# Kernel optimization log

Measured on AMD Instinct MI355X. Metric: run time of the kernel, lower is better.

The kernel has to match this reference:

```python
import jax, jax.numpy as jnp
import numpy as np

EMB_DIM = 768
NUM_HEADS = 12
OUT_DIM = 768


def setup_inputs() -> dict:
    key = jax.random.key(0)
    k_x, k_q, k_k, k_v, k_o = jax.random.split(key, 5)
    B, N, D = 8, 1024, EMB_DIM
    s = 1.0 / np.sqrt(D)
    return {
        "x": jax.random.normal(k_x, (B, N, D), dtype=jnp.float32),
        # torch nn.Linear weights are stored [out_features, in_features]
        "Wq": jax.random.normal(k_q, (D, D), dtype=jnp.float32) * s,
        "Wk": jax.random.normal(k_k, (D, D), dtype=jnp.float32) * s,
        "Wv": jax.random.normal(k_v, (D, D), dtype=jnp.float32) * s,
        "Wo": jax.random.normal(k_o, (OUT_DIM, D), dtype=jnp.float32) * s,
    }


def _split_heads(t, H):
    # [B, N, D] -> [B*H, N, D//H]  (heads folded into batch, per einsum 'b i d')
    B, N, D = t.shape
    return t.reshape(B, N, H, D // H).transpose(0, 2, 1, 3).reshape(B * H, N, D // H)


def _merge_heads(t, B, H):
    BH, N, dh = t.shape
    return t.reshape(B, H, N, dh).transpose(0, 2, 1, 3).reshape(B, N, H * dh)


def reference(x, Wq, Wk, Wv, Wo):
    B, N, D = x.shape
    H = NUM_HEADS
    dh = D // H
    # q/k/v projections (torch Linear: y = x @ W.T, no bias)
    q = _split_heads(x @ Wq.T, H)
    k = _split_heads(x @ Wk.T, H)
    v = _split_heads(x @ Wv.T, H)
    scale = dh ** (-0.5)
    # dots: 'b i d , b j d -> b i j' -> full [B*H, N, N] score matrix
    dots = jnp.einsum('bid,bjd->bij', q, k) * scale
    attn = jax.nn.softmax(dots, axis=-1)
    # dropout p=0.0 -> identity
    # vect: 'b i d , b d j -> b i j' == attn @ v
    vect = jnp.einsum('bij,bjd->bid', attn, v)
    out = _merge_heads(vect, B, H) @ Wo.T
    return out
```

## Files before the change

### kernel.cpp

```cpp
#include <hip/hip_runtime.h>
#include <hip/hip_bf16.h>
#include <stdint.h>


typedef __bf16 bf16x8 __attribute__((ext_vector_type(8)));
typedef float f32x4 __attribute__((ext_vector_type(4)));

#define GAS __attribute__((address_space(1)))
#define LAS __attribute__((address_space(3)))

__device__ __forceinline__ void glds16(const short* gp, short* lp) {
  __builtin_amdgcn_global_load_lds((const GAS void*)gp, (LAS void*)lp, 16, 0, 0);
}

__device__ __forceinline__ short f2bf_bits(float f) {
  union { float f; unsigned u; } cv; cv.f = f;
  unsigned u = cv.u;
  unsigned r = (u + 0x7fffu + ((u >> 16) & 1u)) >> 16;
  return (short)(unsigned short)r;
}

__device__ __forceinline__ void stage8_f32(const float* __restrict__ src, short* dst) {
  float4 f0 = ((const float4*)src)[0];
  float4 f1 = ((const float4*)src)[1];
  short t[8];
  t[0] = f2bf_bits(f0.x); t[1] = f2bf_bits(f0.y);
  t[2] = f2bf_bits(f0.z); t[3] = f2bf_bits(f0.w);
  t[4] = f2bf_bits(f1.x); t[5] = f2bf_bits(f1.y);
  t[6] = f2bf_bits(f1.z); t[7] = f2bf_bits(f1.w);
  *(uint4*)dst = *(const uint4*)t;
}

__global__ __launch_bounds__(256) void convert_kernel(
    const float* __restrict__ x, const float* __restrict__ Wq,
    const float* __restrict__ Wk, const float* __restrict__ Wv,
    short* __restrict__ xb, short* __restrict__ wqkv) {
  int seg = blockIdx.y;
  const float* src; short* dst; int n8;
  if (seg == 0) { src = x; dst = xb; n8 = 786432; }
  else {
    src = (seg == 1) ? Wq : (seg == 2) ? Wk : Wv;
    dst = wqkv + (size_t)(seg - 1) * 589824;
    n8 = 73728;
  }
  int idx = blockIdx.x * 256 + threadIdx.x;
  if (idx >= n8) return;
  stage8_f32(src + (size_t)idx * 8, dst + (size_t)idx * 8);
}

__global__ __launch_bounds__(256) void gemm_qkv(
    const short* __restrict__ xb, const short* __restrict__ wqkv,
    short* __restrict__ q, short* __restrict__ k, short* __restrict__ vt) {
  const int m0 = blockIdx.x * 128;
  const int by = blockIdx.y;
  const int n0g = by * 128;
  const int tid = threadIdx.x;
  const int w = tid >> 6, lane = tid & 63, l16 = lane & 15, quad = lane >> 4;
  const int wr = w >> 1, wc = w & 1;

  __shared__ short sA[128 * 64];
  __shared__ short sB[128 * 64];

  f32x4 acc[4][4];
#pragma unroll
  for (int i = 0; i < 4; ++i)
#pragma unroll
    for (int j = 0; j < 4; ++j) acc[i][j] = (f32x4){0.f, 0.f, 0.f, 0.f};

  for (int k0 = 0; k0 < 768; k0 += 64) {
    __syncthreads();
    const short* Ab = xb + (size_t)m0 * 768 + k0;
    const short* Bb = wqkv + (size_t)n0g * 768 + k0;
#pragma unroll
    for (int p = 0; p < 4; ++p) {
      int lin = (w * 4 + p) * 64 + lane;
      int row = lin >> 3;
      int cs = ((lin & 7) ^ (row & 7)) * 8;
      glds16(Ab + (size_t)row * 768 + cs, &sA[lin * 8]);
      glds16(Bb + (size_t)row * 768 + cs, &sB[lin * 8]);
    }
    __syncthreads();
#pragma unroll
    for (int kk2 = 0; kk2 < 2; ++kk2) {
      bf16x8 af[4], bfg[4];
#pragma unroll
      for (int t = 0; t < 4; ++t) {
        int ra = wr * 64 + t * 16 + l16;
        af[t] = *(const bf16x8*)&sA[ra * 64 + (((kk2 * 4 + quad) ^ (ra & 7)) << 3)];
        int rb = wc * 64 + t * 16 + l16;
        bfg[t] = *(const bf16x8*)&sB[rb * 64 + (((kk2 * 4 + quad) ^ (rb & 7)) << 3)];
      }
#pragma unroll
      for (int ti = 0; ti < 4; ++ti)
#pragma unroll
        for (int tj = 0; tj < 4; ++tj)
          acc[ti][tj] = __builtin_amdgcn_mfma_f32_16x16x32_bf16(af[ti], bfg[tj], acc[ti][tj], 0, 0, 0);
    }
  }

  const int wsel = by / 6;
  const int nl0 = (by % 6) * 128 + wc * 64;
  if (wsel == 2) {
#pragma unroll
    for (int ti = 0; ti < 4; ++ti)
#pragma unroll
      for (int tj = 0; tj < 4; ++tj) {
        int token = m0 + wr * 64 + ti * 16 + quad * 4;
        int nl = nl0 + tj * 16 + l16;
        int bh = (token >> 10) * 12 + (nl >> 6);
        short tmp[4];
#pragma unroll
        for (int r = 0; r < 4; ++r) tmp[r] = f2bf_bits(acc[ti][tj][r]);
        *(uint2*)(vt + (size_t)bh * 65536 + (size_t)(nl & 63) * 1024 + (token & 1023)) =
            *(const uint2*)tmp;
      }
  } else {
    short* C = wsel ? k : q;
#pragma unroll
    for (int ti = 0; ti < 4; ++ti)
#pragma unroll
      for (int tj = 0; tj < 4; ++tj)
#pragma unroll
        for (int r = 0; r < 4; ++r) {
          int row = m0 + wr * 64 + ti * 16 + quad * 4 + r;
          int nl = nl0 + tj * 16 + l16;
          C[(size_t)row * 768 + nl] = f2bf_bits(acc[ti][tj][r]);
        }
  }
}

__global__ __launch_bounds__(256) void attn_kernel(
    const short* __restrict__ q, const short* __restrict__ k,
    const short* __restrict__ vt, short* __restrict__ vect) {
  const int bh = blockIdx.y;
  const int b = bh / 12, h = bh % 12;
  const int m0 = blockIdx.x * 128;
  const int tid = threadIdx.x;
  const int w = tid >> 6, lane = tid & 63, l16 = lane & 15, quad = lane >> 4;

  __shared__ short sQ[128 * 64];
  __shared__ short sK[64 * 64];
  __shared__ short sVt[64 * 64];

  const size_t base = (size_t)b * 786432 + (size_t)h * 64;
  const size_t vbase = (size_t)bh * 65536;

#pragma unroll
  for (int p = 0; p < 4; ++p) {
    int lin = (w * 4 + p) * 64 + lane;
    int row = lin >> 3;
    int cs = ((lin & 7) ^ (row & 7)) * 8;
    glds16(q + base + (size_t)(m0 + row) * 768 + cs, &sQ[lin * 8]);
  }
  __syncthreads();
  bf16x8 bq[2][2];
#pragma unroll
  for (int g = 0; g < 2; ++g)
#pragma unroll
    for (int kk = 0; kk < 2; ++kk) {
      int row = w * 32 + g * 16 + l16;
      bq[g][kk] = *(const bf16x8*)&sQ[row * 64 + (((kk * 4 + quad) ^ (row & 7)) << 3)];
    }

  float l_acc[2] = {0.f, 0.f};
  f32x4 oacc[2][4];
#pragma unroll
  for (int g = 0; g < 2; ++g)
#pragma unroll
    for (int td = 0; td < 4; ++td) oacc[g][td] = (f32x4){0.f, 0.f, 0.f, 0.f};

  for (int j0 = 0; j0 < 1024; j0 += 64) {
    __syncthreads();
#pragma unroll
    for (int p = 0; p < 2; ++p) {
      int lin = (w * 2 + p) * 64 + lane;
      int row = lin >> 3;
      int cs = ((lin & 7) ^ (row & 7)) * 8;
      glds16(k + base + (size_t)(j0 + row) * 768 + cs, &sK[lin * 8]);
      glds16(vt + vbase + (size_t)row * 1024 + j0 + cs, &sVt[lin * 8]);
    }
    __syncthreads();

    f32x4 s[2][4];
#pragma unroll
    for (int g = 0; g < 2; ++g)
#pragma unroll
      for (int ti = 0; ti < 4; ++ti) s[g][ti] = (f32x4){0.f, 0.f, 0.f, 0.f};
#pragma unroll
    for (int kk = 0; kk < 2; ++kk)
#pragma unroll
      for (int ti = 0; ti < 4; ++ti) {
        int row = ti * 16 + l16;
        bf16x8 a = *(const bf16x8*)&sK[row * 64 + (((kk * 4 + quad) ^ (row & 7)) << 3)];
        s[0][ti] = __builtin_amdgcn_mfma_f32_16x16x32_bf16(a, bq[0][kk], s[0][ti], 0, 0, 0);
        s[1][ti] = __builtin_amdgcn_mfma_f32_16x16x32_bf16(a, bq[1][kk], s[1][ti], 0, 0, 0);
      }

    short ps[2][4][4];
#pragma unroll
    for (int g = 0; g < 2; ++g)
#pragma unroll
      for (int ti = 0; ti < 4; ++ti) {
        float p0 = __expf(s[g][ti][0] * 0.125f);
        float p1 = __expf(s[g][ti][1] * 0.125f);
        float p2 = __expf(s[g][ti][2] * 0.125f);
        float p3 = __expf(s[g][ti][3] * 0.125f);
        l_acc[g] += (p0 + p1) + (p2 + p3);
        ps[g][ti][0] = f2bf_bits(p0); ps[g][ti][1] = f2bf_bits(p1);
        ps[g][ti][2] = f2bf_bits(p2); ps[g][ti][3] = f2bf_bits(p3);
      }

#pragma unroll
    for (int t2 = 0; t2 < 2; ++t2) {
      bf16x8 av[4];
#pragma unroll
      for (int td = 0; td < 4; ++td) {
        int row = td * 16 + l16;
        int o1 = t2 * 32 + quad * 4;
        int c1 = o1 >> 3, w1 = o1 & 7;
        int c2 = c1 + 2;
        union { uint2 u[2]; bf16x8 v; } tmp;
        tmp.u[0] = *(const uint2*)&sVt[row * 64 + ((c1 ^ (row & 7)) << 3) + w1];
        tmp.u[1] = *(const uint2*)&sVt[row * 64 + ((c2 ^ (row & 7)) << 3) + w1];
        av[td] = tmp.v;
      }
#pragma unroll
      for (int g = 0; g < 2; ++g) {
        union { short sh[8]; bf16x8 v; } bp;
#pragma unroll
        for (int jj = 0; jj < 4; ++jj) {
          bp.sh[jj] = ps[g][2 * t2][jj];
          bp.sh[4 + jj] = ps[g][2 * t2 + 1][jj];
        }
#pragma unroll
        for (int td = 0; td < 4; ++td)
          oacc[g][td] = __builtin_amdgcn_mfma_f32_16x16x32_bf16(av[td], bp.v, oacc[g][td], 0, 0, 0);
      }
    }
  }

#pragma unroll
  for (int g = 0; g < 2; ++g) {
    float l = l_acc[g];
    l += __shfl_xor(l, 16);
    l += __shfl_xor(l, 32);
    float inv = 1.0f / l;
    int i_tok = m0 + w * 32 + g * 16 + l16;
#pragma unroll
    for (int td = 0; td < 4; ++td) {
      short tmp[4];
#pragma unroll
      for (int r = 0; r < 4; ++r) tmp[r] = f2bf_bits(oacc[g][td][r] * inv);
      *(uint2*)(vect + base + (size_t)i_tok * 768 + td * 16 + quad * 4) = *(const uint2*)tmp;
    }
  }
}

__global__ __launch_bounds__(256) void gemm_out(
    const short* __restrict__ vect, const float* __restrict__ Wo,
    float* __restrict__ out) {
  const int m0 = blockIdx.x * 128;
  const int n0 = blockIdx.y * 128;
  const int tid = threadIdx.x;
  const int w = tid >> 6, lane = tid & 63, l16 = lane & 15, quad = lane >> 4;
  const int wr = w >> 1, wc = w & 1;

  __shared__ short sA[128 * 64];
  __shared__ short sB[128 * 64];

  f32x4 acc[4][4];
#pragma unroll
  for (int i = 0; i < 4; ++i)
#pragma unroll
    for (int j = 0; j < 4; ++j) acc[i][j] = (f32x4){0.f, 0.f, 0.f, 0.f};

  for (int k0 = 0; k0 < 768; k0 += 64) {
    __syncthreads();
    const short* Ab = vect + (size_t)m0 * 768 + k0;
#pragma unroll
    for (int p = 0; p < 4; ++p) {
      int lin = (w * 4 + p) * 64 + lane;
      int row = lin >> 3;
      int cs = ((lin & 7) ^ (row & 7)) * 8;
      glds16(Ab + (size_t)row * 768 + cs, &sA[lin * 8]);
      stage8_f32(Wo + (size_t)(n0 + row) * 768 + k0 + cs, &sB[lin * 8]);
    }
    __syncthreads();
#pragma unroll
    for (int kk2 = 0; kk2 < 2; ++kk2) {
      bf16x8 af[4], bfg[4];
#pragma unroll
      for (int t = 0; t < 4; ++t) {
        int ra = wr * 64 + t * 16 + l16;
        af[t] = *(const bf16x8*)&sA[ra * 64 + (((kk2 * 4 + quad) ^ (ra & 7)) << 3)];
        int rb = wc * 64 + t * 16 + l16;
        bfg[t] = *(const bf16x8*)&sB[rb * 64 + (((kk2 * 4 + quad) ^ (rb & 7)) << 3)];
      }
#pragma unroll
      for (int ti = 0; ti < 4; ++ti)
#pragma unroll
        for (int tj = 0; tj < 4; ++tj)
          acc[ti][tj] = __builtin_amdgcn_mfma_f32_16x16x32_bf16(af[ti], bfg[tj], acc[ti][tj], 0, 0, 0);
    }
  }
#pragma unroll
  for (int ti = 0; ti < 4; ++ti)
#pragma unroll
    for (int tj = 0; tj < 4; ++tj)
#pragma unroll
      for (int r = 0; r < 4; ++r) {
        int row = m0 + wr * 64 + ti * 16 + quad * 4 + r;
        int col = n0 + wc * 64 + tj * 16 + l16;
        out[(size_t)row * 768 + col] = acc[ti][tj][r];
      }
}

extern "C" void kernel_launch(void* const* d_in, const int* in_sizes, int n_in,
                              void* d_out, int out_size, void* d_ws, size_t ws_size,
                              hipStream_t stream) {
  const float* x  = (const float*)d_in[0];
  const float* Wq = (const float*)d_in[1];
  const float* Wk = (const float*)d_in[2];
  const float* Wv = (const float*)d_in[3];
  const float* Wo = (const float*)d_in[4];
  float* out = (float*)d_out;

  const size_t MN = (size_t)8192 * 768;
  short* q    = (short*)d_ws;
  short* k    = q + MN;
  short* vt   = k + MN;
  short* vect = vt + MN;

  short* xb   = (short*)d_out;
  short* wqkv = xb + MN;

  convert_kernel<<<dim3(3072, 4), 256, 0, stream>>>(x, Wq, Wk, Wv, xb, wqkv);
  gemm_qkv<<<dim3(64, 18), 256, 0, stream>>>(xb, wqkv, q, k, vt);
  attn_kernel<<<dim3(8, 96), 256, 0, stream>>>(q, k, vt, vect);
  gemm_out<<<dim3(64, 6), 256, 0, stream>>>(vect, Wo, out);
}
```

Measured before the change: 208.9 us.

## Fold softmax scale into Q, use exp2, native bf16 converts, remap attention grid

Folds the softmax scale and log2(e) into the Q projection epilogue so the attention inner loop can call a raw exp2 builtin instead of a scaled __expf. It replaces the manual round-to-nearest bf16 bit trick with native __bf16 conversions, which may lower to hardware convert instructions. It also keeps the row-sum as a vector accumulator and makes the attention grid 1D with the head index varying fastest, which changes block scheduling and cache locality. Q is now stored pre-scaled in bf16, which slightly changes rounding. There is still no max subtraction, so the kernel relies on the scores being small.

```diff
diff --git a/kernel.cpp b/kernel.cpp
--- a/kernel.cpp
+++ b/kernel.cpp
@@ -4,6 +4,7 @@
 
 
 typedef __bf16 bf16x8 __attribute__((ext_vector_type(8)));
+typedef __bf16 bf16x4 __attribute__((ext_vector_type(4)));
 typedef float f32x4 __attribute__((ext_vector_type(4)));
 
 #define GAS __attribute__((address_space(1)))
@@ -13,22 +14,27 @@
   __builtin_amdgcn_global_load_lds((const GAS void*)gp, (LAS void*)lp, 16, 0, 0);
 }
 
-__device__ __forceinline__ short f2bf_bits(float f) {
-  union { float f; unsigned u; } cv; cv.f = f;
-  unsigned u = cv.u;
-  unsigned r = (u + 0x7fffu + ((u >> 16) & 1u)) >> 16;
-  return (short)(unsigned short)r;
+__device__ __forceinline__ float fast_exp2(float x) {
+#if __has_builtin(__builtin_amdgcn_exp2f)
+  return __builtin_amdgcn_exp2f(x);
+#else
+  return __expf(x * 0.6931471805599453f);
+#endif
+}
+
+__device__ __forceinline__ short bfbits(float f) {
+  __bf16 b = (__bf16)f;
+  union { __bf16 b; short s; } cv; cv.b = b;
+  return cv.s;
 }
 
 __device__ __forceinline__ void stage8_f32(const float* __restrict__ src, short* dst) {
   float4 f0 = ((const float4*)src)[0];
   float4 f1 = ((const float4*)src)[1];
-  short t[8];
-  t[0] = f2bf_bits(f0.x); t[1] = f2bf_bits(f0.y);
-  t[2] = f2bf_bits(f0.z); t[3] = f2bf_bits(f0.w);
-  t[4] = f2bf_bits(f1.x); t[5] = f2bf_bits(f1.y);
-  t[6] = f2bf_bits(f1.z); t[7] = f2bf_bits(f1.w);
-  *(uint4*)dst = *(const uint4*)t;
+  bf16x8 t;
+  t[0] = (__bf16)f0.x; t[1] = (__bf16)f0.y; t[2] = (__bf16)f0.z; t[3] = (__bf16)f0.w;
+  t[4] = (__bf16)f1.x; t[5] = (__bf16)f1.y; t[6] = (__bf16)f1.z; t[7] = (__bf16)f1.w;
+  *(bf16x8*)dst = t;
 }
 
 __global__ __launch_bounds__(256) void convert_kernel(
@@ -110,12 +116,13 @@
         int bh = (token >> 10) * 12 + (nl >> 6);
         short tmp[4];
 #pragma unroll
-        for (int r = 0; r < 4; ++r) tmp[r] = f2bf_bits(acc[ti][tj][r]);
+        for (int r = 0; r < 4; ++r) tmp[r] = bfbits(acc[ti][tj][r]);
         *(uint2*)(vt + (size_t)bh * 65536 + (size_t)(nl & 63) * 1024 + (token & 1023)) =
             *(const uint2*)tmp;
       }
   } else {
     short* C = wsel ? k : q;
+    const float sc = wsel ? 1.0f : 0.1803368801111244f;
 #pragma unroll
     for (int ti = 0; ti < 4; ++ti)
 #pragma unroll
@@ -124,7 +131,7 @@
         for (int r = 0; r < 4; ++r) {
           int row = m0 + wr * 64 + ti * 16 + quad * 4 + r;
           int nl = nl0 + tj * 16 + l16;
-          C[(size_t)row * 768 + nl] = f2bf_bits(acc[ti][tj][r]);
+          C[(size_t)row * 768 + nl] = bfbits(acc[ti][tj][r] * sc);
         }
   }
 }
@@ -132,9 +139,10 @@
 __global__ __launch_bounds__(256) void attn_kernel(
     const short* __restrict__ q, const short* __restrict__ k,
     const short* __restrict__ vt, short* __restrict__ vect) {
-  const int bh = blockIdx.y;
+  const int bh = blockIdx.x % 96;
+  const int qt = blockIdx.x / 96;
   const int b = bh / 12, h = bh % 12;
-  const int m0 = blockIdx.x * 128;
+  const int m0 = qt * 128;
   const int tid = threadIdx.x;
   const int w = tid >> 6, lane = tid & 63, l16 = lane & 15, quad = lane >> 4;
 
@@ -162,12 +170,14 @@
       bq[g][kk] = *(const bf16x8*)&sQ[row * 64 + (((kk * 4 + quad) ^ (row & 7)) << 3)];
     }
 
-  float l_acc[2] = {0.f, 0.f};
+  f32x4 l4[2];
   f32x4 oacc[2][4];
 #pragma unroll
-  for (int g = 0; g < 2; ++g)
+  for (int g = 0; g < 2; ++g) {
+    l4[g] = (f32x4){0.f, 0.f, 0.f, 0.f};
 #pragma unroll
     for (int td = 0; td < 4; ++td) oacc[g][td] = (f32x4){0.f, 0.f, 0.f, 0.f};
+  }
 
   for (int j0 = 0; j0 < 1024; j0 += 64) {
     __syncthreads();
@@ -196,18 +206,21 @@
         s[1][ti] = __builtin_amdgcn_mfma_f32_16x16x32_bf16(a, bq[1][kk], s[1][ti], 0, 0, 0);
       }
 
-    short ps[2][4][4];
+    bf16x4 pb[2][4];
 #pragma unroll
     for (int g = 0; g < 2; ++g)
 #pragma unroll
       for (int ti = 0; ti < 4; ++ti) {
-        float p0 = __expf(s[g][ti][0] * 0.125f);
-        float p1 = __expf(s[g][ti][1] * 0.125f);
-        float p2 = __expf(s[g][ti][2] * 0.125f);
-        float p3 = __expf(s[g][ti][3] * 0.125f);
-        l_acc[g] += (p0 + p1) + (p2 + p3);
-        ps[g][ti][0] = f2bf_bits(p0); ps[g][ti][1] = f2bf_bits(p1);
-        ps[g][ti][2] = f2bf_bits(p2); ps[g][ti][3] = f2bf_bits(p3);
+        f32x4 e;
+        e[0] = fast_exp2(s[g][ti][0]);
+        e[1] = fast_exp2(s[g][ti][1]);
+        e[2] = fast_exp2(s[g][ti][2]);
+        e[3] = fast_exp2(s[g][ti][3]);
+        l4[g] += e;
+        bf16x4 t;
+        t[0] = (__bf16)e[0]; t[1] = (__bf16)e[1];
+        t[2] = (__bf16)e[2]; t[3] = (__bf16)e[3];
+        pb[g][ti] = t;
       }
 
 #pragma unroll
@@ -226,12 +239,9 @@
       }
 #pragma unroll
       for (int g = 0; g < 2; ++g) {
-        union { short sh[8]; bf16x8 v; } bp;
-#pragma unroll
-        for (int jj = 0; jj < 4; ++jj) {
-          bp.sh[jj] = ps[g][2 * t2][jj];
-          bp.sh[4 + jj] = ps[g][2 * t2 + 1][jj];
-        }
+        union { bf16x4 h[2]; bf16x8 v; } bp;
+        bp.h[0] = pb[g][2 * t2];
+        bp.h[1] = pb[g][2 * t2 + 1];
 #pragma unroll
         for (int td = 0; td < 4; ++td)
           oacc[g][td] = __builtin_amdgcn_mfma_f32_16x16x32_bf16(av[td], bp.v, oacc[g][td], 0, 0, 0);
@@ -241,7 +251,7 @@
 
 #pragma unroll
   for (int g = 0; g < 2; ++g) {
-    float l = l_acc[g];
+    float l = (l4[g][0] + l4[g][1]) + (l4[g][2] + l4[g][3]);
     l += __shfl_xor(l, 16);
     l += __shfl_xor(l, 32);
     float inv = 1.0f / l;
@@ -250,7 +260,7 @@
     for (int td = 0; td < 4; ++td) {
       short tmp[4];
 #pragma unroll
-      for (int r = 0; r < 4; ++r) tmp[r] = f2bf_bits(oacc[g][td][r] * inv);
+      for (int r = 0; r < 4; ++r) tmp[r] = bfbits(oacc[g][td][r] * inv);
       *(uint2*)(vect + base + (size_t)i_tok * 768 + td * 16 + quad * 4) = *(const uint2*)tmp;
     }
   }
@@ -336,6 +346,6 @@
 
   convert_kernel<<<dim3(3072, 4), 256, 0, stream>>>(x, Wq, Wk, Wv, xb, wqkv);
   gemm_qkv<<<dim3(64, 18), 256, 0, stream>>>(xb, wqkv, q, k, vt);
-  attn_kernel<<<dim3(8, 96), 256, 0, stream>>>(q, k, vt, vect);
+  attn_kernel<<<768, 256, 0, stream>>>(q, k, vt, vect);
   gemm_out<<<dim3(64, 6), 256, 0, stream>>>(vect, Wo, out);
 }
```

New measurement: 198.8 us. 1.05x faster.
